# Kernel tuning notes

Hardware: AMD Instinct MI355X
Metric: run time of the kernel (lower is better)

## Reference

```python
import jax, jax.numpy as jnp
from jax import lax
import numpy as np

DN = ('NHWC', 'HWIO', 'NHWC')


def setup_inputs() -> dict:
    key = jax.random.key(0)
    ks = jax.random.split(key, 4)
    B, T, H, W, Cin, Cout, K = 4, 16, 64, 64, 32, 64, 3
    x = jax.random.normal(ks[0], (B, T, H, W, Cin), dtype=jnp.float32)
    kernel = jax.random.normal(ks[1], (K, K, Cin, 4 * Cout), dtype=jnp.float32) * 0.05
    rec_kernel = jax.random.normal(ks[2], (K, K, Cout, 4 * Cout), dtype=jnp.float32) * 0.05
    bias = jnp.zeros((4 * Cout,), dtype=jnp.float32)
    gamma = jnp.ones((Cout,), dtype=jnp.float32)
    beta = jnp.zeros((Cout,), dtype=jnp.float32)
    moving_mean = jnp.zeros((Cout,), dtype=jnp.float32)
    moving_var = jnp.ones((Cout,), dtype=jnp.float32)
    return dict(x=x, kernel=kernel, rec_kernel=rec_kernel, bias=bias,
                gamma=gamma, beta=beta, moving_mean=moving_mean, moving_var=moving_var)


def _hard_sigmoid(z):
    # Keras hard_sigmoid: clip(0.2*x + 0.5, 0, 1)
    return jnp.clip(0.2 * z + 0.5, 0.0, 1.0)


def _conv(x, w):
    return lax.conv_general_dilated(x, w, (1, 1), 'SAME', dimension_numbers=DN)


def reference(x, kernel, rec_kernel, bias, gamma, beta, moving_mean, moving_var):
    B, T, H, W, Cin = x.shape
    Cout = rec_kernel.shape[2]
    # Precompute input-to-gate convs for all timesteps at once: (B*T,H,W,4C)
    gx = _conv(x.reshape(B * T, H, W, Cin), kernel) + bias
    gx = gx.reshape(B, T, H, W, 4 * Cout).transpose(1, 0, 2, 3, 4)  # (T,B,H,W,4C)

    def step(carry, gxt):
        h, c = carry
        g = gxt + _conv(h, rec_kernel)  # (B,H,W,4C)
        i, f, cc, o = jnp.split(g, 4, axis=-1)  # Keras gate order i,f,c,o
        i = _hard_sigmoid(i)
        f = _hard_sigmoid(f)
        c = f * c + i * jnp.tanh(cc)
        h = _hard_sigmoid(o) * jnp.tanh(c)
        return (h, c), h

    h0 = jnp.zeros((B, H, W, Cout), dtype=x.dtype)
    c0 = jnp.zeros((B, H, W, Cout), dtype=x.dtype)
    _, hs = lax.scan(step, (h0, c0), gx)  # (T,B,H,W,C)
    y = hs.transpose(1, 0, 2, 3, 4)  # (B,T,H,W,C)
    # BatchNorm, inference mode (training=False), eps=1e-3
    inv = gamma * lax.rsqrt(moving_var + 1e-3)
    return y * inv + (beta - moving_mean * inv)
```

## Files before the change

### kernel.cpp

```cpp
#include <hip/hip_runtime.h>
#include <math.h>

#define B_ 4
#define T_ 16
#define H_ 64
#define W_ 64
#define CIN 32
#define CO 64
#define NG 256
#define PXS 40

typedef __attribute__((ext_vector_type(8))) short bf16x8;
typedef __attribute__((ext_vector_type(4))) float f32x4;

__device__ __forceinline__ float hsig(float z) {
    return fminf(1.f, fmaxf(0.f, 0.2f * z + 0.5f));
}

__device__ __forceinline__ float ftanh(float x) {
    float e = __builtin_amdgcn_exp2f(x * 2.8853900817779268f);
    return 1.f - 2.f * __builtin_amdgcn_rcpf(e + 1.f);
}

__device__ __forceinline__ unsigned short f2bf(float f) {
    union { float f; unsigned u; } v; v.f = f;
    unsigned r = v.u + 0x7FFFu + ((v.u >> 16) & 1u);
    return (unsigned short)(r >> 16);
}

__global__ void transform_weights(const float* __restrict__ wk,
                                  const float* __restrict__ wr,
                                  unsigned short* __restrict__ wkT,
                                  unsigned short* __restrict__ wrT)
{
    int i = blockIdx.x * 256 + threadIdx.x;
    if (i < 9 * 256 * 32) {
        int k = i & 31, n = (i >> 5) & 255, kpos = i >> 13;
        wkT[i] = f2bf(wk[(kpos * 32 + k) * 256 + n]);
    }
    if (i < 9 * 2 * 256 * 32) {
        int k = i & 31, n = (i >> 5) & 255, q = (i >> 13) & 1, kpos = i >> 14;
        wrT[i] = f2bf(wr[(kpos * 64 + q * 32 + k) * 256 + n]);
    }
}

template<bool FIRST>
__global__ __launch_bounds__(768, 3)
void convlstm_step(const float* __restrict__ x,
                   const unsigned short* __restrict__ wkT,
                   const unsigned short* __restrict__ wrT,
                   const float* __restrict__ bias,
                   const float* __restrict__ gamma,
                   const float* __restrict__ beta,
                   const float* __restrict__ mean,
                   const float* __restrict__ var,
                   const unsigned short* __restrict__ hin,
                   unsigned short* __restrict__ hout,
                   float* __restrict__ cbuf,
                   float* __restrict__ out,
                   int t)
{
    __shared__ __align__(16) unsigned short sx[6 * 18 * PXS];
    __shared__ __align__(16) unsigned short shm[2][6 * 18 * PXS];
    __shared__ __align__(16) float axx[4 * 4 * 8 * 256];

    const int tid = threadIdx.x;
    const int wv = tid >> 6, lane = tid & 63;
    const int ln = lane & 15, kg = lane >> 4;
    const int wg = wv >> 2;
    const int sl = wv & 3;

    const int bi = blockIdx.x;
    const int b = bi >> 6, tile = bi & 63;
    const int oy = (tile >> 2) * 4;
    const int ox = (tile & 3) * 16;

    unsigned short* sh0 = shm[0];
    unsigned short* sh1 = shm[1];

    if (wg == 2) {
#pragma unroll
        for (int i = 0; i < 2; ++i) {
            int e = (tid - 512) + i * 256;
            if (e < 432) {
                int c8 = e & 3, p = e >> 2;
                int row = p / 18, col = p - row * 18;
                int gy = oy - 1 + row, gx = ox - 1 + col;
                float4 v0 = make_float4(0.f, 0.f, 0.f, 0.f), v1 = v0;
                if ((unsigned)gy < (unsigned)H_ && (unsigned)gx < (unsigned)W_) {
                    const float* p32 = &x[((((size_t)b * T_ + t) * H_ + gy) * W_ + gx) * CIN + c8 * 8];
                    v0 = *(const float4*)p32; v1 = *(const float4*)(p32 + 4);
                }
                unsigned short* d = &sx[(row * 18 + col) * PXS + c8 * 8];
                d[0] = f2bf(v0.x); d[1] = f2bf(v0.y); d[2] = f2bf(v0.z); d[3] = f2bf(v0.w);
                d[4] = f2bf(v1.x); d[5] = f2bf(v1.y); d[6] = f2bf(v1.z); d[7] = f2bf(v1.w);
            }
        }
    } else if (!FIRST) {
#pragma unroll
        for (int i = 0; i < 2; ++i) {
            int e = tid + i * 512;
            if (e < 864) {
                int o = e & 7, p = e >> 3;
                int row = p / 18, col = p - row * 18;
                int gy = oy - 1 + row, gx = ox - 1 + col;
                uint4 v = make_uint4(0u, 0u, 0u, 0u);
                if ((unsigned)gy < (unsigned)H_ && (unsigned)gx < (unsigned)W_)
                    v = *(const uint4*)&hin[(((size_t)b * H_ + gy) * W_ + gx) * CO + o * 8];
                int q = o >> 2, s4 = o & 3;
                *(uint4*)&shm[q][(row * 18 + col) * PXS + s4 * 8] = v;
            }
        }
    }

    const int ch = sl * 16 + ln;
    const unsigned short* wkp = wkT + (size_t)ch * 32 + kg * 8;
    const unsigned short* wrp = wrT + (size_t)ch * 32 + kg * 8;

    const float bi0 = bias[ch], bi1 = bias[64 + ch], bi2 = bias[128 + ch], bi3 = bias[192 + ch];
    const float inv = gamma[ch] * rsqrtf(var[ch] + 1e-3f);
    const float shift = beta[ch] - mean[ch] * inv;
    float cpv[2][4];
#pragma unroll
    for (int rr = 0; rr < 2; ++rr)
#pragma unroll
        for (int reg = 0; reg < 4; ++reg) cpv[rr][reg] = 0.f;
    if (!FIRST) {
        if (wg == 0) {
#pragma unroll
            for (int reg = 0; reg < 4; ++reg) {
                size_t pix0 = ((size_t)b * H_ + oy + 0) * W_ + (ox + kg * 4 + reg);
                size_t pix1 = ((size_t)b * H_ + oy + 1) * W_ + (ox + kg * 4 + reg);
                cpv[0][reg] = cbuf[pix0 * CO + ch];
                cpv[1][reg] = cbuf[pix1 * CO + ch];
            }
        } else {
            const int r = (wg == 1) ? 2 : 3;
#pragma unroll
            for (int reg = 0; reg < 4; ++reg) {
                size_t pix = ((size_t)b * H_ + oy + r) * W_ + (ox + kg * 4 + reg);
                cpv[0][reg] = cbuf[pix * CO + ch];
            }
        }
    }

    __syncthreads();

    f32x4 acc[4][4];
#pragma unroll
    for (int g = 0; g < 4; ++g)
#pragma unroll
        for (int r = 0; r < 4; ++r) acc[g][r] = (f32x4){0.f, 0.f, 0.f, 0.f};

#define WPTR(c) ((c) < 9 ? (wkp + (size_t)(c) * 8192) : (wrp + (size_t)((c) - 9) * 8192))
#define SRCB(c) ((c) < 9 ? sx : ((((c) - 9) & 1) ? sh1 : sh0))
#define KP(c)   ((c) < 9 ? (c) : (((c) - 9) >> 1))

#define CHUNK(c) {                                                               \
    const unsigned short* wp_ = WPTR(c);                                         \
    bf16x8 w0 = *(const bf16x8*)(wp_);                                           \
    bf16x8 w1 = *(const bf16x8*)(wp_ + 2048);                                    \
    bf16x8 w2 = *(const bf16x8*)(wp_ + 4096);                                    \
    bf16x8 w3 = *(const bf16x8*)(wp_ + 6144);                                    \
    const int ky_ = KP(c) / 3, kx_ = KP(c) - (KP(c) / 3) * 3;                    \
    const unsigned short* sb_ = SRCB(c);                                         \
    bf16x8 a0 = *(const bf16x8*)&sb_[((0 + ky_) * 18 + ln + kx_) * PXS + kg * 8];\
    bf16x8 a1 = *(const bf16x8*)&sb_[((1 + ky_) * 18 + ln + kx_) * PXS + kg * 8];\
    bf16x8 a2 = *(const bf16x8*)&sb_[((2 + ky_) * 18 + ln + kx_) * PXS + kg * 8];\
    bf16x8 a3 = *(const bf16x8*)&sb_[((3 + ky_) * 18 + ln + kx_) * PXS + kg * 8];\
    __builtin_amdgcn_s_setprio(1);                                               \
    acc[0][0] = __builtin_amdgcn_mfma_f32_16x16x32_bf16(a0, w0, acc[0][0], 0, 0, 0); \
    acc[0][1] = __builtin_amdgcn_mfma_f32_16x16x32_bf16(a1, w0, acc[0][1], 0, 0, 0); \
    acc[0][2] = __builtin_amdgcn_mfma_f32_16x16x32_bf16(a2, w0, acc[0][2], 0, 0, 0); \
    acc[0][3] = __builtin_amdgcn_mfma_f32_16x16x32_bf16(a3, w0, acc[0][3], 0, 0, 0); \
    acc[1][0] = __builtin_amdgcn_mfma_f32_16x16x32_bf16(a0, w1, acc[1][0], 0, 0, 0); \
    acc[1][1] = __builtin_amdgcn_mfma_f32_16x16x32_bf16(a1, w1, acc[1][1], 0, 0, 0); \
    acc[1][2] = __builtin_amdgcn_mfma_f32_16x16x32_bf16(a2, w1, acc[1][2], 0, 0, 0); \
    acc[1][3] = __builtin_amdgcn_mfma_f32_16x16x32_bf16(a3, w1, acc[1][3], 0, 0, 0); \
    acc[2][0] = __builtin_amdgcn_mfma_f32_16x16x32_bf16(a0, w2, acc[2][0], 0, 0, 0); \
    acc[2][1] = __builtin_amdgcn_mfma_f32_16x16x32_bf16(a1, w2, acc[2][1], 0, 0, 0); \
    acc[2][2] = __builtin_amdgcn_mfma_f32_16x16x32_bf16(a2, w2, acc[2][2], 0, 0, 0); \
    acc[2][3] = __builtin_amdgcn_mfma_f32_16x16x32_bf16(a3, w2, acc[2][3], 0, 0, 0); \
    acc[3][0] = __builtin_amdgcn_mfma_f32_16x16x32_bf16(a0, w3, acc[3][0], 0, 0, 0); \
    acc[3][1] = __builtin_amdgcn_mfma_f32_16x16x32_bf16(a1, w3, acc[3][1], 0, 0, 0); \
    acc[3][2] = __builtin_amdgcn_mfma_f32_16x16x32_bf16(a2, w3, acc[3][2], 0, 0, 0); \
    acc[3][3] = __builtin_amdgcn_mfma_f32_16x16x32_bf16(a3, w3, acc[3][3], 0, 0, 0); \
    __builtin_amdgcn_s_setprio(0); }

    if (wg == 0) {
        CHUNK(0) CHUNK(1) CHUNK(2) CHUNK(3) CHUNK(4) CHUNK(5) CHUNK(6) CHUNK(7) CHUNK(8)
    } else if (wg == 1) {
        if (!FIRST) {
            CHUNK(9) CHUNK(10) CHUNK(11) CHUNK(12) CHUNK(13) CHUNK(14) CHUNK(15) CHUNK(16) CHUNK(17)
        }
    } else {
        if (!FIRST) {
            CHUNK(18) CHUNK(19) CHUNK(20) CHUNK(21) CHUNK(22) CHUNK(23) CHUNK(24) CHUNK(25) CHUNK(26)
        }
    }

    const int axo = (ln << 4) + (kg << 2);
#define AXPUB(s, G, R) *(f32x4*)&axx[(((sl * 4 + (G)) * 8 + (s)) << 8) + axo] = acc[G][R];
#define AXRD(s, G)     (*(const f32x4*)&axx[(((sl * 4 + (G)) * 8 + (s)) << 8) + axo])

    if (wg == 0) {
#pragma unroll
        for (int g = 0; g < 4; ++g) { AXPUB(4, g, 2) AXPUB(6, g, 3) }
    } else if (wg == 1) {
#pragma unroll
        for (int g = 0; g < 4; ++g) { AXPUB(0, g, 0) AXPUB(2, g, 1) AXPUB(7, g, 3) }
    } else {
#pragma unroll
        for (int g = 0; g < 4; ++g) { AXPUB(1, g, 0) AXPUB(3, g, 1) AXPUB(5, g, 2) }
    }
    __syncthreads();

#define EPI(R, CPI, S0, S1) {                                                    \
        const int gy = oy + (R);                                                 \
        f32x4 av[4];                                                             \
        _Pragma("unroll")                                                        \
        for (int g = 0; g < 4; ++g)                                              \
            av[g] = acc[g][R] + AXRD(S0, g) + AXRD(S1, g);                       \
        _Pragma("unroll")                                                        \
        for (int reg = 0; reg < 4; ++reg) {                                      \
            const int gx = ox + kg * 4 + reg;                                    \
            size_t pix = ((size_t)b * H_ + gy) * W_ + gx;                        \
            float ig = hsig(av[0][reg] + bi0);                                   \
            float fg = hsig(av[1][reg] + bi1);                                   \
            float cg = ftanh(av[2][reg] + bi2);                                  \
            float og = hsig(av[3][reg] + bi3);                                   \
            float cv = fg * cpv[CPI][reg] + ig * cg;                             \
            float hv = og * ftanh(cv);                                           \
            cbuf[pix * CO + ch] = cv;                                            \
            hout[pix * CO + ch] = f2bf(hv);                                      \
            __builtin_nontemporal_store(hv * inv + shift,                        \
                &out[((((size_t)b * T_ + t) * H_ + gy) * W_ + gx) * CO + ch]);   \
        }                                                                        \
    }

    if (wg == 0)      { EPI(0, 0, 0, 1) EPI(1, 1, 2, 3) }
    else if (wg == 1) { EPI(2, 0, 4, 5) }
    else              { EPI(3, 0, 6, 7) }
#undef EPI
#undef AXPUB
#undef AXRD
#undef CHUNK
#undef WPTR
#undef SRCB
#undef KP
}

extern "C" void kernel_launch(void* const* d_in, const int* in_sizes, int n_in,
                              void* d_out, int out_size, void* d_ws, size_t ws_size,
                              hipStream_t stream)
{
    (void)in_sizes; (void)n_in; (void)out_size; (void)ws_size;
    const float* x     = (const float*)d_in[0];
    const float* wk    = (const float*)d_in[1];
    const float* wr    = (const float*)d_in[2];
    const float* bias  = (const float*)d_in[3];
    const float* gamma = (const float*)d_in[4];
    const float* beta  = (const float*)d_in[5];
    const float* mean  = (const float*)d_in[6];
    const float* var   = (const float*)d_in[7];
    float* out = (float*)d_out;

    const size_t plane = (size_t)B_ * H_ * W_ * CO;
    unsigned short* h0 = (unsigned short*)d_ws;
    unsigned short* h1 = h0 + plane;
    float* cb = (float*)(h1 + plane);
    unsigned short* wkT = (unsigned short*)(cb + plane);
    unsigned short* wrT = wkT + 9 * 256 * 32;

    transform_weights<<<576, 256, 0, stream>>>(wk, wr, wkT, wrT);

    for (int t = 0; t < T_; ++t) {
        const unsigned short* hin = (t & 1) ? h0 : h1;
        unsigned short* houtp     = (t & 1) ? h1 : h0;
        if (t == 0)
            convlstm_step<true><<<256, 768, 0, stream>>>(x, wkT, wrT, bias, gamma, beta, mean, var,
                                                         hin, houtp, cb, out, t);
        else
            convlstm_step<false><<<256, 768, 0, stream>>>(x, wkT, wrT, bias, gamma, beta, mean, var,
                                                          hin, houtp, cb, out, t);
    }
}
```

Measured before the change: 294.9 us.

## Fuse all timesteps into one persistent kernel with neighbor-flag synchronization

Replaces the sixteen per-timestep launches with one persistent kernel. Each block loops over time, keeps its cell state in registers, and waits only on flags published by its eight neighbouring tiles before reading their halo of h, using coherent loads and stores. This removes launch overhead, global barriers between steps, and the round trip of the c buffer through global memory. It adds spin-waiting and uncached coherent traffic, and it relies on all 256 blocks being resident at once to avoid deadlock.

Result: slower. 508.5 us (+72.4%).

```diff
diff --git a/kernel.cpp b/kernel.cpp
--- a/kernel.cpp
+++ b/kernel.cpp
@@ -7,7 +7,6 @@
 #define W_ 64
 #define CIN 32
 #define CO 64
-#define NG 256
 #define PXS 40
 
 typedef __attribute__((ext_vector_type(8))) short bf16x8;
@@ -28,10 +27,23 @@
     return (unsigned short)(r >> 16);
 }
 
+__device__ __forceinline__ uint4 ldg_coh16(const unsigned short* p) {
+    uint4 v;
+    asm volatile("global_load_dwordx4 %0, %1, off sc0 sc1\n\t"
+                 "s_waitcnt vmcnt(0)"
+                 : "=v"(v) : "v"(p) : "memory");
+    return v;
+}
+__device__ __forceinline__ void stg_coh16b(unsigned short* p, unsigned short d) {
+    unsigned dd = d;
+    asm volatile("global_store_short %0, %1, off sc0 sc1" :: "v"(p), "v"(dd) : "memory");
+}
+
 __global__ void transform_weights(const float* __restrict__ wk,
                                   const float* __restrict__ wr,
                                   unsigned short* __restrict__ wkT,
-                                  unsigned short* __restrict__ wrT)
+                                  unsigned short* __restrict__ wrT,
+                                  int* __restrict__ flags)
 {
     int i = blockIdx.x * 256 + threadIdx.x;
     if (i < 9 * 256 * 32) {
@@ -42,23 +54,22 @@
         int k = i & 31, n = (i >> 5) & 255, q = (i >> 13) & 1, kpos = i >> 14;
         wrT[i] = f2bf(wr[(kpos * 64 + q * 32 + k) * 256 + n]);
     }
-}
-
-template<bool FIRST>
+    if (i < 256 * 16) flags[i] = 0;
+}
+
 __global__ __launch_bounds__(768, 3)
-void convlstm_step(const float* __restrict__ x,
-                   const unsigned short* __restrict__ wkT,
-                   const unsigned short* __restrict__ wrT,
-                   const float* __restrict__ bias,
-                   const float* __restrict__ gamma,
-                   const float* __restrict__ beta,
-                   const float* __restrict__ mean,
-                   const float* __restrict__ var,
-                   const unsigned short* __restrict__ hin,
-                   unsigned short* __restrict__ hout,
-                   float* __restrict__ cbuf,
-                   float* __restrict__ out,
-                   int t)
+void convlstm_persist(const float* __restrict__ x,
+                      const unsigned short* __restrict__ wkT,
+                      const unsigned short* __restrict__ wrT,
+                      const float* __restrict__ bias,
+                      const float* __restrict__ gamma,
+                      const float* __restrict__ beta,
+                      const float* __restrict__ mean,
+                      const float* __restrict__ var,
+                      unsigned short* __restrict__ h0,
+                      unsigned short* __restrict__ h1,
+                      int* __restrict__ flags,
+                      float* __restrict__ out)
 {
     __shared__ __align__(16) unsigned short sx[6 * 18 * PXS];
     __shared__ __align__(16) unsigned short shm[2][6 * 18 * PXS];
@@ -72,46 +83,21 @@
 
     const int bi = blockIdx.x;
     const int b = bi >> 6, tile = bi & 63;
-    const int oy = (tile >> 2) * 4;
-    const int ox = (tile & 3) * 16;
+    const int ty = tile >> 2, tx = tile & 3;
+    const int oy = ty * 4, ox = tx * 16;
 
     unsigned short* sh0 = shm[0];
     unsigned short* sh1 = shm[1];
 
-    if (wg == 2) {
-#pragma unroll
-        for (int i = 0; i < 2; ++i) {
-            int e = (tid - 512) + i * 256;
-            if (e < 432) {
-                int c8 = e & 3, p = e >> 2;
-                int row = p / 18, col = p - row * 18;
-                int gy = oy - 1 + row, gx = ox - 1 + col;
-                float4 v0 = make_float4(0.f, 0.f, 0.f, 0.f), v1 = v0;
-                if ((unsigned)gy < (unsigned)H_ && (unsigned)gx < (unsigned)W_) {
-                    const float* p32 = &x[((((size_t)b * T_ + t) * H_ + gy) * W_ + gx) * CIN + c8 * 8];
-                    v0 = *(const float4*)p32; v1 = *(const float4*)(p32 + 4);
-                }
-                unsigned short* d = &sx[(row * 18 + col) * PXS + c8 * 8];
-                d[0] = f2bf(v0.x); d[1] = f2bf(v0.y); d[2] = f2bf(v0.z); d[3] = f2bf(v0.w);
-                d[4] = f2bf(v1.x); d[5] = f2bf(v1.y); d[6] = f2bf(v1.z); d[7] = f2bf(v1.w);
-            }
-        }
-    } else if (!FIRST) {
-#pragma unroll
-        for (int i = 0; i < 2; ++i) {
-            int e = tid + i * 512;
-            if (e < 864) {
-                int o = e & 7, p = e >> 3;
-                int row = p / 18, col = p - row * 18;
-                int gy = oy - 1 + row, gx = ox - 1 + col;
-                uint4 v = make_uint4(0u, 0u, 0u, 0u);
-                if ((unsigned)gy < (unsigned)H_ && (unsigned)gx < (unsigned)W_)
-                    v = *(const uint4*)&hin[(((size_t)b * H_ + gy) * W_ + gx) * CO + o * 8];
-                int q = o >> 2, s4 = o & 3;
-                *(uint4*)&shm[q][(row * 18 + col) * PXS + s4 * 8] = v;
-            }
-        }
-    }
+    int* nbf = nullptr;
+    if (tid < 8) {
+        int k = tid + (tid >= 4 ? 1 : 0);
+        int dy = k / 3 - 1, dx = k - (k / 3) * 3 - 1;
+        int ny = ty + dy, nx = tx + dx;
+        if (ny >= 0 && ny < 16 && nx >= 0 && nx < 4)
+            nbf = flags + ((b * 64 + ny * 4 + nx) << 4);
+    }
+    int* myflag = flags + (bi << 4);
 
     const int ch = sl * 16 + ln;
     const unsigned short* wkp = wkT + (size_t)ch * 32 + kg * 8;
@@ -120,37 +106,66 @@
     const float bi0 = bias[ch], bi1 = bias[64 + ch], bi2 = bias[128 + ch], bi3 = bias[192 + ch];
     const float inv = gamma[ch] * rsqrtf(var[ch] + 1e-3f);
     const float shift = beta[ch] - mean[ch] * inv;
+
     float cpv[2][4];
 #pragma unroll
     for (int rr = 0; rr < 2; ++rr)
 #pragma unroll
         for (int reg = 0; reg < 4; ++reg) cpv[rr][reg] = 0.f;
-    if (!FIRST) {
-        if (wg == 0) {
-#pragma unroll
-            for (int reg = 0; reg < 4; ++reg) {
-                size_t pix0 = ((size_t)b * H_ + oy + 0) * W_ + (ox + kg * 4 + reg);
-                size_t pix1 = ((size_t)b * H_ + oy + 1) * W_ + (ox + kg * 4 + reg);
-                cpv[0][reg] = cbuf[pix0 * CO + ch];
-                cpv[1][reg] = cbuf[pix1 * CO + ch];
-            }
-        } else {
-            const int r = (wg == 1) ? 2 : 3;
-#pragma unroll
-            for (int reg = 0; reg < 4; ++reg) {
-                size_t pix = ((size_t)b * H_ + oy + r) * W_ + (ox + kg * 4 + reg);
-                cpv[0][reg] = cbuf[pix * CO + ch];
-            }
-        }
-    }
-
-    __syncthreads();
-
-    f32x4 acc[4][4];
-#pragma unroll
-    for (int g = 0; g < 4; ++g)
-#pragma unroll
-        for (int r = 0; r < 4; ++r) acc[g][r] = (f32x4){0.f, 0.f, 0.f, 0.f};
+
+#pragma unroll 1
+    for (int t = 0; t < T_; ++t) {
+        const unsigned short* hinp = (t & 1) ? h0 : h1;
+        unsigned short* houtp      = (t & 1) ? h1 : h0;
+
+        if (wg == 2) {
+#pragma unroll
+            for (int i = 0; i < 2; ++i) {
+                int e = (tid - 512) + i * 256;
+                if (e < 432) {
+                    int c8 = e & 3, p = e >> 2;
+                    int row = p / 18, col = p - row * 18;
+                    int gy = oy - 1 + row, gx = ox - 1 + col;
+                    float4 v0 = make_float4(0.f, 0.f, 0.f, 0.f), v1 = v0;
+                    if ((unsigned)gy < (unsigned)H_ && (unsigned)gx < (unsigned)W_) {
+                        const float* p32 = &x[((((size_t)b * T_ + t) * H_ + gy) * W_ + gx) * CIN + c8 * 8];
+                        v0 = *(const float4*)p32; v1 = *(const float4*)(p32 + 4);
+                    }
+                    unsigned short* d = &sx[(row * 18 + col) * PXS + c8 * 8];
+                    d[0] = f2bf(v0.x); d[1] = f2bf(v0.y); d[2] = f2bf(v0.z); d[3] = f2bf(v0.w);
+                    d[4] = f2bf(v1.x); d[5] = f2bf(v1.y); d[6] = f2bf(v1.z); d[7] = f2bf(v1.w);
+                }
+            }
+        }
+        if (t > 0 && nbf) {
+            while (__hip_atomic_load(nbf, __ATOMIC_RELAXED, __HIP_MEMORY_SCOPE_AGENT) < t)
+                __builtin_amdgcn_s_sleep(2);
+        }
+        __syncthreads();
+
+        if (t > 0 && wg < 2) {
+#pragma unroll
+            for (int i = 0; i < 2; ++i) {
+                int e = tid + i * 512;
+                if (e < 864) {
+                    int o = e & 7, p = e >> 3;
+                    int row = p / 18, col = p - row * 18;
+                    int gy = oy - 1 + row, gx = ox - 1 + col;
+                    uint4 v = make_uint4(0u, 0u, 0u, 0u);
+                    if ((unsigned)gy < (unsigned)H_ && (unsigned)gx < (unsigned)W_)
+                        v = ldg_coh16(&hinp[(((size_t)b * H_ + gy) * W_ + gx) * CO + o * 8]);
+                    int q = o >> 2, s4 = o & 3;
+                    *(uint4*)&shm[q][(row * 18 + col) * PXS + s4 * 8] = v;
+                }
+            }
+        }
+        __syncthreads();
+
+        f32x4 acc[4][4];
+#pragma unroll
+        for (int g = 0; g < 4; ++g)
+#pragma unroll
+            for (int r = 0; r < 4; ++r) acc[g][r] = (f32x4){0.f, 0.f, 0.f, 0.f};
 
 #define WPTR(c) ((c) < 9 ? (wkp + (size_t)(c) * 8192) : (wrp + (size_t)((c) - 9) * 8192))
 #define SRCB(c) ((c) < 9 ? sx : ((((c) - 9) & 1) ? sh1 : sh0))
@@ -187,33 +202,33 @@
     acc[3][3] = __builtin_amdgcn_mfma_f32_16x16x32_bf16(a3, w3, acc[3][3], 0, 0, 0); \
     __builtin_amdgcn_s_setprio(0); }
 
-    if (wg == 0) {
-        CHUNK(0) CHUNK(1) CHUNK(2) CHUNK(3) CHUNK(4) CHUNK(5) CHUNK(6) CHUNK(7) CHUNK(8)
-    } else if (wg == 1) {
-        if (!FIRST) {
-            CHUNK(9) CHUNK(10) CHUNK(11) CHUNK(12) CHUNK(13) CHUNK(14) CHUNK(15) CHUNK(16) CHUNK(17)
-        }
-    } else {
-        if (!FIRST) {
-            CHUNK(18) CHUNK(19) CHUNK(20) CHUNK(21) CHUNK(22) CHUNK(23) CHUNK(24) CHUNK(25) CHUNK(26)
-        }
-    }
-
-    const int axo = (ln << 4) + (kg << 2);
+        if (wg == 0) {
+            CHUNK(0) CHUNK(1) CHUNK(2) CHUNK(3) CHUNK(4) CHUNK(5) CHUNK(6) CHUNK(7) CHUNK(8)
+        } else if (wg == 1) {
+            if (t > 0) {
+                CHUNK(9) CHUNK(10) CHUNK(11) CHUNK(12) CHUNK(13) CHUNK(14) CHUNK(15) CHUNK(16) CHUNK(17)
+            }
+        } else {
+            if (t > 0) {
+                CHUNK(18) CHUNK(19) CHUNK(20) CHUNK(21) CHUNK(22) CHUNK(23) CHUNK(24) CHUNK(25) CHUNK(26)
+            }
+        }
+
+        const int axo = (ln << 4) + (kg << 2);
 #define AXPUB(s, G, R) *(f32x4*)&axx[(((sl * 4 + (G)) * 8 + (s)) << 8) + axo] = acc[G][R];
 #define AXRD(s, G)     (*(const f32x4*)&axx[(((sl * 4 + (G)) * 8 + (s)) << 8) + axo])
 
-    if (wg == 0) {
-#pragma unroll
-        for (int g = 0; g < 4; ++g) { AXPUB(4, g, 2) AXPUB(6, g, 3) }
-    } else if (wg == 1) {
-#pragma unroll
-        for (int g = 0; g < 4; ++g) { AXPUB(0, g, 0) AXPUB(2, g, 1) AXPUB(7, g, 3) }
-    } else {
-#pragma unroll
-        for (int g = 0; g < 4; ++g) { AXPUB(1, g, 0) AXPUB(3, g, 1) AXPUB(5, g, 2) }
-    }
-    __syncthreads();
+        if (wg == 0) {
+#pragma unroll
+            for (int g = 0; g < 4; ++g) { AXPUB(4, g, 2) AXPUB(6, g, 3) }
+        } else if (wg == 1) {
+#pragma unroll
+            for (int g = 0; g < 4; ++g) { AXPUB(0, g, 0) AXPUB(2, g, 1) AXPUB(7, g, 3) }
+        } else {
+#pragma unroll
+            for (int g = 0; g < 4; ++g) { AXPUB(1, g, 0) AXPUB(3, g, 1) AXPUB(5, g, 2) }
+        }
+        __syncthreads();
 
 #define EPI(R, CPI, S0, S1) {                                                    \
         const int gy = oy + (R);                                                 \
@@ -230,17 +245,17 @@
             float cg = ftanh(av[2][reg] + bi2);                                  \
             float og = hsig(av[3][reg] + bi3);                                   \
             float cv = fg * cpv[CPI][reg] + ig * cg;                             \
+            cpv[CPI][reg] = cv;                                                  \
             float hv = og * ftanh(cv);                                           \
-            cbuf[pix * CO + ch] = cv;                                            \
-            hout[pix * CO + ch] = f2bf(hv);                                      \
+            stg_coh16b(&houtp[pix * CO + ch], f2bf(hv));                         \
             __builtin_nontemporal_store(hv * inv + shift,                        \
                 &out[((((size_t)b * T_ + t) * H_ + gy) * W_ + gx) * CO + ch]);   \
         }                                                                        \
     }
 
-    if (wg == 0)      { EPI(0, 0, 0, 1) EPI(1, 1, 2, 3) }
-    else if (wg == 1) { EPI(2, 0, 4, 5) }
-    else              { EPI(3, 0, 6, 7) }
+        if (wg == 0)      { EPI(0, 0, 0, 1) EPI(1, 1, 2, 3) }
+        else if (wg == 1) { EPI(2, 0, 4, 5) }
+        else              { EPI(3, 0, 6, 7) }
 #undef EPI
 #undef AXPUB
 #undef AXRD
@@ -248,6 +263,11 @@
 #undef WPTR
 #undef SRCB
 #undef KP
+
+        __syncthreads();
+        if (tid == 0)
+            __hip_atomic_store(myflag, t + 1, __ATOMIC_RELAXED, __HIP_MEMORY_SCOPE_AGENT);
+    }
 }
 
 extern "C" void kernel_launch(void* const* d_in, const int* in_sizes, int n_in,
@@ -268,20 +288,11 @@
     const size_t plane = (size_t)B_ * H_ * W_ * CO;
     unsigned short* h0 = (unsigned short*)d_ws;
     unsigned short* h1 = h0 + plane;
-    float* cb = (float*)(h1 + plane);
-    unsigned short* wkT = (unsigned short*)(cb + plane);
+    unsigned short* wkT = h1 + plane;
     unsigned short* wrT = wkT + 9 * 256 * 32;
-
-    transform_weights<<<576, 256, 0, stream>>>(wk, wr, wkT, wrT);
-
-    for (int t = 0; t < T_; ++t) {
-        const unsigned short* hin = (t & 1) ? h0 : h1;
-        unsigned short* houtp     = (t & 1) ? h1 : h0;
-        if (t == 0)
-            convlstm_step<true><<<256, 768, 0, stream>>>(x, wkT, wrT, bias, gamma, beta, mean, var,
-                                                         hin, houtp, cb, out, t);
-        else
-            convlstm_step<false><<<256, 768, 0, stream>>>(x, wkT, wrT, bias, gamma, beta, mean, var,
-                                                          hin, houtp, cb, out, t);
-    }
-}
+    int* flags = (int*)(wrT + 9 * 2 * 256 * 32);
+
+    transform_weights<<<576, 256, 0, stream>>>(wk, wr, wkT, wrT, flags);
+    convlstm_persist<<<256, 768, 0, stream>>>(x, wkT, wrT, bias, gamma, beta, mean, var,
+                                              h0, h1, flags, out);
+}
```
